# Performance work log

Hardware: AMD Instinct MI355X
Metric: run time of the kernel (lower is better)

Reference implementation:

```python
import jax, jax.numpy as jnp
import numpy as np

N = 50000          # nodes
E = 1000000        # edges (k=20 avg degree)
SD = 32            # scalar_dim = hidden_dim//2
VD = 32            # vector_dim = hidden_dim//2
L = 3              # num_layers
SPIN = 2           # spin_symmetry
IN_DIM = 2 * SD + VD + 3   # message MLP input dim = 99
OUT_DIM = SD + VD          # 64


def setup_inputs() -> dict:
    key = jax.random.key(0)
    ks = jax.random.split(key, 12)
    pos = jax.random.uniform(ks[0], (N, 2), dtype=jnp.float32)
    redshift = jax.random.uniform(ks[1], (N, 1), dtype=jnp.float32)
    input_shapes = jax.random.normal(ks[2], (N, 2), dtype=jnp.float32)
    edge_index = jax.random.randint(ks[3], (2, E), 0, N, dtype=jnp.int64)
    # encoder params
    enc_s_w = jax.random.normal(ks[4], (SD, 1), dtype=jnp.float32) * 0.5
    enc_s_b = jax.random.normal(ks[5], (SD,), dtype=jnp.float32) * 0.1
    enc_v_w = jax.random.normal(ks[6], (VD, 2), dtype=jnp.float32) * 0.5
    # per-layer message MLP params, stacked over layers
    W1 = jax.random.normal(ks[7], (L, OUT_DIM, IN_DIM), dtype=jnp.float32) * (1.0 / np.sqrt(IN_DIM))
    b1 = jax.random.normal(ks[8], (L, OUT_DIM), dtype=jnp.float32) * 0.1
    W2 = jax.random.normal(ks[9], (L, OUT_DIM, OUT_DIM), dtype=jnp.float32) * (1.0 / np.sqrt(OUT_DIM))
    b2 = jax.random.normal(ks[10], (L, OUT_DIM), dtype=jnp.float32) * 0.1
    return {"pos": pos, "redshift": redshift, "input_shapes": input_shapes,
            "edge_index": edge_index, "enc_s_w": enc_s_w, "enc_s_b": enc_s_b,
            "enc_v_w": enc_v_w, "W1": W1, "b1": b1, "W2": W2, "b2": b2}


def _frame_layer(h_s, h_v, pos, orientation, src, dst, W1, b1, W2, b2):
    # per-edge geometric features
    dpos = pos[src] - pos[dst]                                   # [E,2]
    dist = jnp.sqrt(jnp.sum(dpos * dpos, axis=1)) + 1e-6          # [E]
    phi_global = jnp.arctan2(dpos[:, 1], dpos[:, 0])              # [E]
    alpha_i = orientation[dst, 0]                                 # [E]
    delta_phi = phi_global - alpha_i
    geo = jnp.stack([dist, jnp.cos(SPIN * delta_phi), jnp.sin(SPIN * delta_phi)], axis=-1)  # [E,3]
    # rotate source vector features into destination local frame
    beta_j = orientation[src, 0]
    rot = (beta_j - alpha_i) * SPIN
    c, s = jnp.cos(rot)[:, None], jnp.sin(rot)[:, None]           # [E,1]
    v_j = h_v[src].reshape(-1, VD // 2, 2)                        # [E,nv,2]
    vx = v_j[..., 0] * c - v_j[..., 1] * s
    vy = v_j[..., 0] * s + v_j[..., 1] * c
    v_rot = jnp.stack([vx, vy], axis=-1).reshape(-1, VD)          # [E,VD]
    # message MLP
    msg_in = jnp.concatenate([h_s[src], h_s[dst], v_rot, geo], axis=-1)  # [E,IN_DIM]
    hid = jax.nn.silu(msg_in @ W1.T + b1)
    raw = hid @ W2.T + b2                                         # [E,OUT_DIM]
    msg_s, msg_v = raw[:, :SD], raw[:, SD:]
    # scatter-add to destination nodes
    out_s = jax.ops.segment_sum(msg_s, dst, num_segments=h_s.shape[0])
    out_v = jax.ops.segment_sum(msg_v, dst, num_segments=h_v.shape[0])
    return h_s + out_s, h_v + out_v


def reference(pos, redshift, input_shapes, edge_index, enc_s_w, enc_s_b, enc_v_w, W1, b1, W2, b2):
    src, dst = edge_index[0], edge_index[1]
    h_s = jax.nn.relu(redshift @ enc_s_w.T + enc_s_b)             # [N,SD]
    h_v = input_shapes @ enc_v_w.T                                # [N,VD]
    orientation = jnp.zeros((pos.shape[0], 1), dtype=pos.dtype)
    for l in range(L):
        h_s, h_v = _frame_layer(h_s, h_v, pos, orientation, src, dst,
                                W1[l], b1[l], W2[l], b2[l])
    return h_s, h_v
```

## Files before the change

kernel.cpp:

```cpp
#include <hip/hip_runtime.h>
#include <hip/hip_bf16.h>

#define WPB 4
#define TILE 16

typedef unsigned short ushort_t;
typedef unsigned int uint_t;

__device__ __forceinline__ float silu_f(float x) {
  return x * __builtin_amdgcn_rcpf(1.0f + __expf(-x));
}
__device__ __forceinline__ int rfl(int x) { return __builtin_amdgcn_readfirstlane(x); }
__device__ __forceinline__ float readlane_f(float v, int l) {
  return __int_as_float(__builtin_amdgcn_readlane(__float_as_int(v), l));
}
__device__ __forceinline__ ushort_t f2bf(float f) {
  uint_t u = __float_as_uint(f);
  u += 0x7FFFu + ((u >> 16) & 1u);
  return (ushort_t)(u >> 16);
}
__device__ __forceinline__ float bf2f(ushort_t b) {
  return __uint_as_float(((uint_t)b) << 16);
}

__global__ void encode_kernel(const float* __restrict__ redshift,
                              const float* __restrict__ shapes,
                              const float* __restrict__ enc_s_w,
                              const float* __restrict__ enc_s_b,
                              const float* __restrict__ enc_v_w,
                              float* __restrict__ hout, int N_) {
  int tid = blockIdx.x * blockDim.x + threadIdx.x;
  int n = tid >> 5;
  int j = tid & 31;
  if (n >= N_) return;
  float r = redshift[n];
  float hs = fmaxf(fmaf(r, enc_s_w[j], enc_s_b[j]), 0.0f);
  float x0 = shapes[n * 2 + 0];
  float x1 = shapes[n * 2 + 1];
  float hv = fmaf(x0, enc_v_w[j * 2 + 0], x1 * enc_v_w[j * 2 + 1]);
  hout[(size_t)n * 32 + j] = hs;
  hout[(size_t)N_ * 32 + (size_t)n * 32 + j] = hv;
}

__global__ void zero_kernel(int* __restrict__ p, int n) {
  int i = blockIdx.x * blockDim.x + threadIdx.x;
  if (i < n) p[i] = 0;
}

__global__ void deg_kernel(const int* __restrict__ ei, int* __restrict__ deg, int E_) {
  int e = blockIdx.x * blockDim.x + threadIdx.x;
  if (e < E_) atomicAdd(&deg[ei[E_ + e]], 1);
}

__global__ __launch_bounds__(1024) void scanA_kernel(const int* __restrict__ deg,
                                                     int* __restrict__ rowptr,
                                                     int* __restrict__ bsum, int n) {
  __shared__ int wsum[16];
  int t = threadIdx.x, lane = t & 63, wid = t >> 6;
  int i = blockIdx.x * 1024 + t;
  int v = (i < n) ? deg[i] : 0;
  int x = v;
#pragma unroll
  for (int off = 1; off < 64; off <<= 1) {
    int y = __shfl_up(x, off);
    if (lane >= off) x += y;
  }
  if (lane == 63) wsum[wid] = x;
  __syncthreads();
  if (t == 0) {
    int run = 0;
#pragma unroll
    for (int w = 0; w < 16; ++w) { int s = wsum[w]; wsum[w] = run; run += s; }
  }
  __syncthreads();
  int inc = x + wsum[wid];
  if (i < n) rowptr[i + 1] = inc;
  if (t == 1023) bsum[blockIdx.x] = inc;
}

__global__ __launch_bounds__(1024) void scanB_kernel(int* __restrict__ bsum, int nb) {
  __shared__ int wsum[16];
  int t = threadIdx.x, lane = t & 63, wid = t >> 6;
  int v = (t < nb) ? bsum[t] : 0;
  int x = v;
#pragma unroll
  for (int off = 1; off < 64; off <<= 1) {
    int y = __shfl_up(x, off);
    if (lane >= off) x += y;
  }
  if (lane == 63) wsum[wid] = x;
  __syncthreads();
  if (t == 0) {
    int run = 0;
#pragma unroll
    for (int w = 0; w < 16; ++w) { int s = wsum[w]; wsum[w] = run; run += s; }
  }
  __syncthreads();
  if (t < nb) bsum[t] = x - v + wsum[wid];
}

__global__ void scanC_kernel(int* __restrict__ rowptr, const int* __restrict__ bsum, int n) {
  int i = blockIdx.x * blockDim.x + threadIdx.x;
  if (i == 0) rowptr[0] = 0;
  if (i < n) rowptr[i + 1] += bsum[i >> 10];
}

__global__ void scatter_kernel(const int* __restrict__ ei, const float* __restrict__ pos,
                               const int* __restrict__ rowptr, int* __restrict__ cursor,
                               float4* __restrict__ edata, int* __restrict__ dstS,
                               int E_, int padE, int N_) {
  int e = blockIdx.x * blockDim.x + threadIdx.x;
  if (e >= padE) return;
  if (e >= E_) {
    edata[e] = make_float4(0.f, 0.f, 0.f, __int_as_float(0));
    dstS[e] = N_;
    return;
  }
  int s = ei[e];
  int d = ei[E_ + e];
  int idx = rowptr[d] + atomicAdd(&cursor[d], 1);
  float dx = pos[s * 2 + 0] - pos[d * 2 + 0];
  float dy = pos[s * 2 + 1] - pos[d * 2 + 1];
  float r2 = fmaf(dx, dx, dy * dy);
  float dist = sqrtf(r2) + 1e-6f;
  float c2 = 1.0f, s2 = 0.0f;
  if (r2 > 0.0f) {
    float inv = 1.0f / r2;
    c2 = (dx * dx - dy * dy) * inv;
    s2 = 2.0f * dx * dy * inv;
  }
  edata[idx] = make_float4(dist, c2, s2, __int_as_float(s));
  dstS[idx] = d;
}

__global__ __launch_bounds__(256) void psd_kernel(
    const float* __restrict__ hout, const float* __restrict__ W1l,
    const float* __restrict__ b1l,
    ushort_t* __restrict__ PSh, ushort_t* __restrict__ PDBh,
    float* __restrict__ H, int N_) {
  __shared__ float wsh[99 * 64];
  __shared__ __align__(16) float hsh[TILE][64];
  int t = threadIdx.x;
  for (int i = t; i < 99 * 64; i += 256) wsh[i] = W1l[i];
  __syncthreads();
  int lane = t & 63, wib = t >> 6;
  float ws_[32], wd_[32], wv_[32];
#pragma unroll
  for (int k = 0; k < 32; ++k) {
    ws_[k] = wsh[lane * 99 + k];
    wd_[k] = wsh[lane * 99 + 32 + k];
    wv_[k] = wsh[lane * 99 + 64 + k];
  }
  float bb1 = b1l[lane];
  const int nTiles = (N_ + TILE - 1) / TILE;
  const float* hvbase = hout + (size_t)N_ * 32;
  int tt = t & 127;
  int sn = tt >> 3;
  int sc = tt & 7;
  for (int tile = blockIdx.x; tile < nTiles; tile += gridDim.x) {
    int base = tile * TILE;
    {
      int n = base + sn;
      const float* src = (t < 128) ? (hout + (size_t)n * 32 + sc * 4)
                                   : (hvbase + (size_t)n * 32 + sc * 4);
      float4 v = (n < N_) ? *reinterpret_cast<const float4*>(src)
                          : make_float4(0.f, 0.f, 0.f, 0.f);
      *reinterpret_cast<float4*>(&hsh[sn][(t < 128 ? 0 : 32) + sc * 4]) = v;
    }
    __syncthreads();
#pragma unroll
    for (int q = 0; q < 4; ++q) {
      int r = wib + q * 4;
      int n = base + r;
      if (n < N_) {
        const float4* ha = reinterpret_cast<const float4*>(hsh[r]);
        float ps0 = 0.f, ps1 = 0.f, ps2 = 0.f, ps3 = 0.f, pd0 = 0.f, pd1 = 0.f;
#pragma unroll
        for (int k4 = 0; k4 < 8; ++k4) {
          float4 a = ha[k4];
          float4 v = ha[8 + k4];
          int k = k4 * 4;
          ps0 = fmaf(a.x, ws_[k], ps0);     pd0 = fmaf(a.x, wd_[k], pd0);
          ps1 = fmaf(a.y, ws_[k + 1], ps1); pd1 = fmaf(a.y, wd_[k + 1], pd1);
          ps2 = fmaf(a.z, ws_[k + 2], ps2); pd0 = fmaf(a.z, wd_[k + 2], pd0);
          ps3 = fmaf(a.w, ws_[k + 3], ps3); pd1 = fmaf(a.w, wd_[k + 3], pd1);
          ps0 = fmaf(v.x, wv_[k], ps0);
          ps1 = fmaf(v.y, wv_[k + 1], ps1);
          ps2 = fmaf(v.z, wv_[k + 2], ps2);
          ps3 = fmaf(v.w, wv_[k + 3], ps3);
        }
        PSh[(size_t)n * 64 + lane] = f2bf((ps0 + ps1) + (ps2 + ps3));
        PDBh[(size_t)n * 64 + lane] = f2bf((pd0 + pd1) + bb1);
        H[(size_t)n * 64 + lane] = 0.0f;
      }
    }
    __syncthreads();
  }
}

__global__ __launch_bounds__(256) void edge_kernel(
    const ushort_t* __restrict__ PSh, const ushort_t* __restrict__ PDBh,
    const float4* __restrict__ edata, const int* __restrict__ dstS,
    const float* __restrict__ W1l, float* __restrict__ H, int nchunk) {
  int lane = threadIdx.x & 63, wib = threadIdx.x >> 6;
  int chunk = blockIdx.x * WPB + wib;
  if (chunk >= nchunk) return;
  int base = chunk << 6;
  float wg0 = W1l[lane * 99 + 96];
  float wg1 = W1l[lane * 99 + 97];
  float wg2 = W1l[lane * 99 + 98];
  float4 ed = edata[base + lane];
  int dv = dstS[base + lane];
  int sv = __float_as_int(ed.w);
  int dprev = __shfl_up(dv, 1);
  unsigned long long bmask = __ballot(dv != dprev) & ~1ull;
  int dcur = rfl(dv);
  float pdj = bf2f(PDBh[(size_t)dcur * 64 + lane]);
  int bnext = bmask ? (int)__builtin_ctzll(bmask) : 64;
  int dnext = (bnext < 64) ? __builtin_amdgcn_readlane(dv, bnext) : dcur;
  float pdj_next = bf2f(PDBh[(size_t)dnext * 64 + lane]);
  float acc0 = 0.0f, acc1 = 0.0f;
#pragma unroll
  for (int e = 0; e < 64; ++e) {
    if (e == bnext) {
      atomicAdd(H + (size_t)dcur * 64 + lane, acc0 + acc1);
      acc0 = acc1 = 0.0f;
      dcur = dnext;
      pdj = pdj_next;
      bmask &= bmask - 1;
      bnext = bmask ? (int)__builtin_ctzll(bmask) : 64;
      dnext = (bnext < 64) ? __builtin_amdgcn_readlane(dv, bnext) : dcur;
      pdj_next = bf2f(PDBh[(size_t)dnext * 64 + lane]);
    }
    int se = __builtin_amdgcn_readlane(sv, e);
    float di = readlane_f(ed.x, e);
    float c2 = readlane_f(ed.y, e);
    float s2 = readlane_f(ed.z, e);
    float ps = bf2f(PSh[(size_t)se * 64 + lane]);
    float pre = fmaf(wg0, di, fmaf(wg1, c2, fmaf(wg2, s2, ps + pdj)));
    if (e & 1) acc1 += silu_f(pre); else acc0 += silu_f(pre);
  }
  atomicAdd(H + (size_t)dcur * 64 + lane, acc0 + acc1);
}

__global__ __launch_bounds__(256) void updproj_kernel(
    float* __restrict__ hout, float* __restrict__ H,
    const int* __restrict__ deg,
    const float* __restrict__ W2l, const float* __restrict__ b2l,
    const float* __restrict__ W1n, const float* __restrict__ b1n,
    ushort_t* __restrict__ PSh, ushort_t* __restrict__ PDBh, int N_) {
  __shared__ float w2sh[64 * 65];
  __shared__ float wsh[99 * 64];
  __shared__ __align__(16) float Hsh[TILE][64];
  int t = threadIdx.x;
  for (int i = t; i < 64 * 64; i += 256) w2sh[(i >> 6) * 65 + (i & 63)] = W2l[i];
  for (int i = t; i < 99 * 64; i += 256) wsh[i] = W1n[i];
  __syncthreads();
  int lane = t & 63, wib = t >> 6;
  float w2[64];
#pragma unroll
  for (int k = 0; k < 64; ++k) w2[k] = w2sh[lane * 65 + k];
  float ws_[32], wd_[32], wv_[32];
#pragma unroll
  for (int k = 0; k < 32; ++k) {
    ws_[k] = wsh[lane * 99 + k];
    wd_[k] = wsh[lane * 99 + 32 + k];
    wv_[k] = wsh[lane * 99 + 64 + k];
  }
  float bb2 = b2l[lane];
  float bb1 = b1n[lane];
  const int nTiles = (N_ + TILE - 1) / TILE;
  size_t plane = (size_t)(lane >> 5) * ((size_t)N_ * 32);
  int sn = t >> 4;
  int sc = t & 15;
  for (int tile = blockIdx.x; tile < nTiles; tile += gridDim.x) {
    int base = tile * TILE;
    {
      int n = base + sn;
      float4 v = (n < N_) ? *reinterpret_cast<const float4*>(H + (size_t)n * 64 + sc * 4)
                          : make_float4(0.f, 0.f, 0.f, 0.f);
      *reinterpret_cast<float4*>(&Hsh[sn][sc * 4]) = v;
    }
    __syncthreads();
#pragma unroll
    for (int q = 0; q < 4; ++q) {
      int r = wib + q * 4;
      int n = base + r;
      if (n < N_) {
        const float4* hm = reinterpret_cast<const float4*>(Hsh[r]);
        float o0 = 0.f, o1 = 0.f;
#pragma unroll
        for (int k4 = 0; k4 < 16; k4 += 2) {
          float4 m0 = hm[k4];
          float4 m1 = hm[k4 + 1];
          o0 = fmaf(m0.x, w2[k4 * 4 + 0], o0);
          o0 = fmaf(m0.y, w2[k4 * 4 + 1], o0);
          o0 = fmaf(m0.z, w2[k4 * 4 + 2], o0);
          o0 = fmaf(m0.w, w2[k4 * 4 + 3], o0);
          o1 = fmaf(m1.x, w2[k4 * 4 + 4], o1);
          o1 = fmaf(m1.y, w2[k4 * 4 + 5], o1);
          o1 = fmaf(m1.z, w2[k4 * 4 + 6], o1);
          o1 = fmaf(m1.w, w2[k4 * 4 + 7], o1);
        }
        float degf = (float)deg[n];
        size_t idx = plane + (size_t)n * 32 + (lane & 31);
        float hnew = hout[idx] + (o0 + o1) + degf * bb2;
        hout[idx] = hnew;
        Hsh[r][lane] = hnew;
        asm volatile("s_waitcnt lgkmcnt(0)" ::: "memory");
        const float4* ha = reinterpret_cast<const float4*>(Hsh[r]);
        float ps0 = 0.f, ps1 = 0.f, ps2 = 0.f, ps3 = 0.f, pd0 = 0.f, pd1 = 0.f;
#pragma unroll
        for (int k4 = 0; k4 < 8; ++k4) {
          float4 a = ha[k4];
          float4 v = ha[8 + k4];
          int k = k4 * 4;
          ps0 = fmaf(a.x, ws_[k], ps0);     pd0 = fmaf(a.x, wd_[k], pd0);
          ps1 = fmaf(a.y, ws_[k + 1], ps1); pd1 = fmaf(a.y, wd_[k + 1], pd1);
          ps2 = fmaf(a.z, ws_[k + 2], ps2); pd0 = fmaf(a.z, wd_[k + 2], pd0);
          ps3 = fmaf(a.w, ws_[k + 3], ps3); pd1 = fmaf(a.w, wd_[k + 3], pd1);
          ps0 = fmaf(v.x, wv_[k], ps0);
          ps1 = fmaf(v.y, wv_[k + 1], ps1);
          ps2 = fmaf(v.z, wv_[k + 2], ps2);
          ps3 = fmaf(v.w, wv_[k + 3], ps3);
        }
        PSh[(size_t)n * 64 + lane] = f2bf((ps0 + ps1) + (ps2 + ps3));
        PDBh[(size_t)n * 64 + lane] = f2bf((pd0 + pd1) + bb1);
        H[(size_t)n * 64 + lane] = 0.0f;
      }
    }
    __syncthreads();
  }
}

__global__ __launch_bounds__(256) void out_kernel(
    float* __restrict__ hout, const float* __restrict__ H,
    const int* __restrict__ deg,
    const float* __restrict__ W2l, const float* __restrict__ b2l, int N_) {
  __shared__ float w2sh[64 * 65];
  __shared__ __align__(16) float Hsh[TILE][64];
  int t = threadIdx.x;
  for (int i = t; i < 64 * 64; i += 256) w2sh[(i >> 6) * 65 + (i & 63)] = W2l[i];
  __syncthreads();
  int lane = t & 63, wib = t >> 6;
  float w2[64];
#pragma unroll
  for (int k = 0; k < 64; ++k) w2[k] = w2sh[lane * 65 + k];
  float bb2 = b2l[lane];
  const int nTiles = (N_ + TILE - 1) / TILE;
  size_t plane = (size_t)(lane >> 5) * ((size_t)N_ * 32);
  int sn = t >> 4;
  int sc = t & 15;
  for (int tile = blockIdx.x; tile < nTiles; tile += gridDim.x) {
    int base = tile * TILE;
    {
      int n = base + sn;
      float4 v = (n < N_) ? *reinterpret_cast<const float4*>(H + (size_t)n * 64 + sc * 4)
                          : make_float4(0.f, 0.f, 0.f, 0.f);
      *reinterpret_cast<float4*>(&Hsh[sn][sc * 4]) = v;
    }
    __syncthreads();
#pragma unroll
    for (int q = 0; q < 4; ++q) {
      int r = wib + q * 4;
      int n = base + r;
      if (n < N_) {
        const float4* hm = reinterpret_cast<const float4*>(Hsh[r]);
        float o0 = 0.f, o1 = 0.f;
#pragma unroll
        for (int k4 = 0; k4 < 16; k4 += 2) {
          float4 m0 = hm[k4];
          float4 m1 = hm[k4 + 1];
          o0 = fmaf(m0.x, w2[k4 * 4 + 0], o0);
          o0 = fmaf(m0.y, w2[k4 * 4 + 1], o0);
          o0 = fmaf(m0.z, w2[k4 * 4 + 2], o0);
          o0 = fmaf(m0.w, w2[k4 * 4 + 3], o0);
          o1 = fmaf(m1.x, w2[k4 * 4 + 4], o1);
          o1 = fmaf(m1.y, w2[k4 * 4 + 5], o1);
          o1 = fmaf(m1.z, w2[k4 * 4 + 6], o1);
          o1 = fmaf(m1.w, w2[k4 * 4 + 7], o1);
        }
        float degf = (float)deg[n];
        size_t idx = plane + (size_t)n * 32 + (lane & 31);
        hout[idx] += (o0 + o1) + degf * bb2;
      }
    }
    __syncthreads();
  }
}

extern "C" void kernel_launch(void* const* d_in, const int* in_sizes, int n_in,
                              void* d_out, int out_size, void* d_ws, size_t ws_size,
                              hipStream_t stream) {
  const float* pos      = (const float*)d_in[0];
  const float* redshift = (const float*)d_in[1];
  const float* shapes   = (const float*)d_in[2];
  const int*   ei       = (const int*)d_in[3];
  const float* enc_s_w  = (const float*)d_in[4];
  const float* enc_s_b  = (const float*)d_in[5];
  const float* enc_v_w  = (const float*)d_in[6];
  const float* W1       = (const float*)d_in[7];
  const float* b1       = (const float*)d_in[8];
  const float* W2       = (const float*)d_in[9];
  const float* b2       = (const float*)d_in[10];

  const int N_ = in_sizes[1];
  const int E_ = in_sizes[3] / 2;
  const int nchunk = (E_ + 63) / 64;
  const int padE = nchunk * 64;

  float4*   edata = (float4*)d_ws;
  float*    H     = (float*)(edata + padE);
  ushort_t* PSh   = (ushort_t*)(H + (size_t)(N_ + 1) * 64);
  ushort_t* PDBh  = PSh + (size_t)N_ * 64;
  int* dstS   = (int*)(PDBh + (size_t)(N_ + 1) * 64);
  int* rowptr = dstS + padE;
  int* deg    = rowptr + (N_ + 1);
  int* cursor = deg + N_;
  int* bsum   = cursor + N_;

  float* hout = (float*)d_out;

  encode_kernel<<<dim3((N_ * 32 + 255) / 256), dim3(256), 0, stream>>>(
      redshift, shapes, enc_s_w, enc_s_b, enc_v_w, hout, N_);

  zero_kernel<<<dim3((2 * N_ + 255) / 256), dim3(256), 0, stream>>>(deg, 2 * N_);
  deg_kernel<<<dim3((E_ + 255) / 256), dim3(256), 0, stream>>>(ei, deg, E_);
  const int nbA = (N_ + 1023) / 1024;
  scanA_kernel<<<dim3(nbA), dim3(1024), 0, stream>>>(deg, rowptr, bsum, N_);
  scanB_kernel<<<dim3(1), dim3(1024), 0, stream>>>(bsum, nbA);
  scanC_kernel<<<dim3((N_ + 255) / 256), dim3(256), 0, stream>>>(rowptr, bsum, N_);
  scatter_kernel<<<dim3((padE + 255) / 256), dim3(256), 0, stream>>>(
      ei, pos, rowptr, cursor, edata, dstS, E_, padE, N_);

  const int edgeBlocks = (nchunk + WPB - 1) / WPB;

  psd_kernel<<<dim3(1024), dim3(256), 0, stream>>>(
      hout, W1, b1, PSh, PDBh, H, N_);

  for (int l = 0; l < 3; ++l) {
    const float* W2l = W2 + (size_t)l * 64 * 64;
    const float* b2l = b2 + (size_t)l * 64;
    edge_kernel<<<dim3(edgeBlocks), dim3(256), 0, stream>>>(
        PSh, PDBh, edata, dstS, W1 + (size_t)l * 64 * 99, H, nchunk);
    if (l < 2) {
      updproj_kernel<<<dim3(1024), dim3(256), 0, stream>>>(
          hout, H, deg, W2l, b2l,
          W1 + (size_t)(l + 1) * 64 * 99, b1 + (size_t)(l + 1) * 64,
          PSh, PDBh, N_);
    } else {
      out_kernel<<<dim3(1024), dim3(256), 0, stream>>>(
          hout, H, deg, W2l, b2l, N_);
    }
  }
}
```

Baseline: 401.7 us.

## Pack edge data into one float4 and batch source-row gathers by eight

Stores cos/sin of the edge angle as two bf16 values in one word, so the float4 per edge now carries dist, packed trig, source and destination. This removes the separate dstS array and its load in the edge kernel. The edge loop is also restructured to issue eight PSh gathers up front per group, giving more memory-level parallelism. In exchange the angle features lose precision to bf16 and the eight prefetched values raise register pressure.

Measured after the change: 324.7 us. 1.24x faster.

```diff
diff --git a/kernel.cpp b/kernel.cpp
--- a/kernel.cpp
+++ b/kernel.cpp
@@ -107,13 +107,12 @@
 
 __global__ void scatter_kernel(const int* __restrict__ ei, const float* __restrict__ pos,
                                const int* __restrict__ rowptr, int* __restrict__ cursor,
-                               float4* __restrict__ edata, int* __restrict__ dstS,
+                               float4* __restrict__ edata,
                                int E_, int padE, int N_) {
   int e = blockIdx.x * blockDim.x + threadIdx.x;
   if (e >= padE) return;
   if (e >= E_) {
-    edata[e] = make_float4(0.f, 0.f, 0.f, __int_as_float(0));
-    dstS[e] = N_;
+    edata[e] = make_float4(0.f, 0.f, __int_as_float(0), __int_as_float(N_));
     return;
   }
   int s = ei[e];
@@ -129,8 +128,9 @@
     c2 = (dx * dx - dy * dy) * inv;
     s2 = 2.0f * dx * dy * inv;
   }
-  edata[idx] = make_float4(dist, c2, s2, __int_as_float(s));
-  dstS[idx] = d;
+  uint_t pk = ((uint_t)f2bf(s2) << 16) | (uint_t)f2bf(c2);
+  edata[idx] = make_float4(dist, __uint_as_float(pk),
+                           __int_as_float(s), __int_as_float(d));
 }
 
 __global__ __launch_bounds__(256) void psd_kernel(
@@ -200,7 +200,7 @@
 
 __global__ __launch_bounds__(256) void edge_kernel(
     const ushort_t* __restrict__ PSh, const ushort_t* __restrict__ PDBh,
-    const float4* __restrict__ edata, const int* __restrict__ dstS,
+    const float4* __restrict__ edata,
     const float* __restrict__ W1l, float* __restrict__ H, int nchunk) {
   int lane = threadIdx.x & 63, wib = threadIdx.x >> 6;
   int chunk = blockIdx.x * WPB + wib;
@@ -210,8 +210,8 @@
   float wg1 = W1l[lane * 99 + 97];
   float wg2 = W1l[lane * 99 + 98];
   float4 ed = edata[base + lane];
-  int dv = dstS[base + lane];
-  int sv = __float_as_int(ed.w);
+  int sv = __float_as_int(ed.z);
+  int dv = __float_as_int(ed.w);
   int dprev = __shfl_up(dv, 1);
   unsigned long long bmask = __ballot(dv != dprev) & ~1ull;
   int dcur = rfl(dv);
@@ -221,24 +221,49 @@
   float pdj_next = bf2f(PDBh[(size_t)dnext * 64 + lane]);
   float acc0 = 0.0f, acc1 = 0.0f;
 #pragma unroll
-  for (int e = 0; e < 64; ++e) {
-    if (e == bnext) {
-      atomicAdd(H + (size_t)dcur * 64 + lane, acc0 + acc1);
-      acc0 = acc1 = 0.0f;
-      dcur = dnext;
-      pdj = pdj_next;
-      bmask &= bmask - 1;
-      bnext = bmask ? (int)__builtin_ctzll(bmask) : 64;
-      dnext = (bnext < 64) ? __builtin_amdgcn_readlane(dv, bnext) : dcur;
-      pdj_next = bf2f(PDBh[(size_t)dnext * 64 + lane]);
-    }
-    int se = __builtin_amdgcn_readlane(sv, e);
-    float di = readlane_f(ed.x, e);
-    float c2 = readlane_f(ed.y, e);
-    float s2 = readlane_f(ed.z, e);
-    float ps = bf2f(PSh[(size_t)se * 64 + lane]);
-    float pre = fmaf(wg0, di, fmaf(wg1, c2, fmaf(wg2, s2, ps + pdj)));
-    if (e & 1) acc1 += silu_f(pre); else acc0 += silu_f(pre);
+  for (int g = 0; g < 8; ++g) {
+    float ps0, ps1, ps2, ps3, ps4, ps5, ps6, ps7;
+    {
+      int s0 = __builtin_amdgcn_readlane(sv, g * 8 + 0);
+      int s1 = __builtin_amdgcn_readlane(sv, g * 8 + 1);
+      int s2_ = __builtin_amdgcn_readlane(sv, g * 8 + 2);
+      int s3 = __builtin_amdgcn_readlane(sv, g * 8 + 3);
+      int s4 = __builtin_amdgcn_readlane(sv, g * 8 + 4);
+      int s5 = __builtin_amdgcn_readlane(sv, g * 8 + 5);
+      int s6 = __builtin_amdgcn_readlane(sv, g * 8 + 6);
+      int s7 = __builtin_amdgcn_readlane(sv, g * 8 + 7);
+      ps0 = bf2f(PSh[(size_t)s0 * 64 + lane]);
+      ps1 = bf2f(PSh[(size_t)s1 * 64 + lane]);
+      ps2 = bf2f(PSh[(size_t)s2_ * 64 + lane]);
+      ps3 = bf2f(PSh[(size_t)s3 * 64 + lane]);
+      ps4 = bf2f(PSh[(size_t)s4 * 64 + lane]);
+      ps5 = bf2f(PSh[(size_t)s5 * 64 + lane]);
+      ps6 = bf2f(PSh[(size_t)s6 * 64 + lane]);
+      ps7 = bf2f(PSh[(size_t)s7 * 64 + lane]);
+    }
+#pragma unroll
+    for (int i = 0; i < 8; ++i) {
+      int e = g * 8 + i;
+      if (e == bnext) {
+        atomicAdd(H + (size_t)dcur * 64 + lane, acc0 + acc1);
+        acc0 = acc1 = 0.0f;
+        dcur = dnext;
+        pdj = pdj_next;
+        bmask &= bmask - 1;
+        bnext = bmask ? (int)__builtin_ctzll(bmask) : 64;
+        dnext = (bnext < 64) ? __builtin_amdgcn_readlane(dv, bnext) : dcur;
+        pdj_next = bf2f(PDBh[(size_t)dnext * 64 + lane]);
+      }
+      float psv = (i == 0) ? ps0 : (i == 1) ? ps1 : (i == 2) ? ps2 :
+                  (i == 3) ? ps3 : (i == 4) ? ps4 : (i == 5) ? ps5 :
+                  (i == 6) ? ps6 : ps7;
+      float di = readlane_f(ed.x, e);
+      uint_t pk = (uint_t)__builtin_amdgcn_readlane(__float_as_int(ed.y), e);
+      float c2 = __uint_as_float(pk << 16);
+      float s2 = __uint_as_float(pk & 0xFFFF0000u);
+      float pre = fmaf(wg0, di, fmaf(wg1, c2, fmaf(wg2, s2, psv + pdj)));
+      if (e & 1) acc1 += silu_f(pre); else acc0 += silu_f(pre);
+    }
   }
   atomicAdd(H + (size_t)dcur * 64 + lane, acc0 + acc1);
 }
@@ -413,8 +438,7 @@
   float*    H     = (float*)(edata + padE);
   ushort_t* PSh   = (ushort_t*)(H + (size_t)(N_ + 1) * 64);
   ushort_t* PDBh  = PSh + (size_t)N_ * 64;
-  int* dstS   = (int*)(PDBh + (size_t)(N_ + 1) * 64);
-  int* rowptr = dstS + padE;
+  int* rowptr = (int*)(PDBh + (size_t)(N_ + 1) * 64);
   int* deg    = rowptr + (N_ + 1);
   int* cursor = deg + N_;
   int* bsum   = cursor + N_;
@@ -431,7 +455,7 @@
   scanB_kernel<<<dim3(1), dim3(1024), 0, stream>>>(bsum, nbA);
   scanC_kernel<<<dim3((N_ + 255) / 256), dim3(256), 0, stream>>>(rowptr, bsum, N_);
   scatter_kernel<<<dim3((padE + 255) / 256), dim3(256), 0, stream>>>(
-      ei, pos, rowptr, cursor, edata, dstS, E_, padE, N_);
+      ei, pos, rowptr, cursor, edata, E_, padE, N_);
 
   const int edgeBlocks = (nchunk + WPB - 1) / WPB;
 
@@ -442,7 +466,7 @@
     const float* W2l = W2 + (size_t)l * 64 * 64;
     const float* b2l = b2 + (size_t)l * 64;
     edge_kernel<<<dim3(edgeBlocks), dim3(256), 0, stream>>>(
-        PSh, PDBh, edata, dstS, W1 + (size_t)l * 64 * 99, H, nchunk);
+        PSh, PDBh, edata, W1 + (size_t)l * 64 * 99, H, nchunk);
     if (l < 2) {
       updproj_kernel<<<dim3(1024), dim3(256), 0, stream>>>(
           hout, H, deg, W2l, b2l,
```

## Replace CSR build with bucket sort and software-pipeline edge gathers

Applied to the files above, without the earlier changes.

The degree count, three-pass scan and atomic scatter are replaced by a two-level bucket sort. Edges go into fixed-capacity sub-buckets of 256 destination nodes, and each bucket is then sorted locally in shared memory; degrees come from the local histogram. Edge records are packed into one float4 (dist, bf16 cos/sin pair, src, dst), which removes the separate dst array. The edge kernel now issues source-row gathers in double-buffered groups of eight so memory latency overlaps with SiLU accumulation. In exchange, the fixed bucket capacity assumes roughly uniform destinations and could overflow on skewed graphs, and the geometry terms lose precision to bf16.

Measured after the change: 421.7 us. 5.0% more time.

```diff
diff --git a/kernel.cpp b/kernel.cpp
--- a/kernel.cpp
+++ b/kernel.cpp
@@ -3,6 +3,8 @@
 
 #define WPB 4
 #define TILE 16
+#define SUBB 8
+#define BCAP 896
 
 typedef unsigned short ushort_t;
 typedef unsigned int uint_t;
@@ -47,78 +49,13 @@
   if (i < n) p[i] = 0;
 }
 
-__global__ void deg_kernel(const int* __restrict__ ei, int* __restrict__ deg, int E_) {
+__global__ void bucket_kernel(const int* __restrict__ ei, const float* __restrict__ pos,
+                              int* __restrict__ bcnt, float4* __restrict__ bdata,
+                              int E_) {
   int e = blockIdx.x * blockDim.x + threadIdx.x;
-  if (e < E_) atomicAdd(&deg[ei[E_ + e]], 1);
-}
-
-__global__ __launch_bounds__(1024) void scanA_kernel(const int* __restrict__ deg,
-                                                     int* __restrict__ rowptr,
-                                                     int* __restrict__ bsum, int n) {
-  __shared__ int wsum[16];
-  int t = threadIdx.x, lane = t & 63, wid = t >> 6;
-  int i = blockIdx.x * 1024 + t;
-  int v = (i < n) ? deg[i] : 0;
-  int x = v;
-#pragma unroll
-  for (int off = 1; off < 64; off <<= 1) {
-    int y = __shfl_up(x, off);
-    if (lane >= off) x += y;
-  }
-  if (lane == 63) wsum[wid] = x;
-  __syncthreads();
-  if (t == 0) {
-    int run = 0;
-#pragma unroll
-    for (int w = 0; w < 16; ++w) { int s = wsum[w]; wsum[w] = run; run += s; }
-  }
-  __syncthreads();
-  int inc = x + wsum[wid];
-  if (i < n) rowptr[i + 1] = inc;
-  if (t == 1023) bsum[blockIdx.x] = inc;
-}
-
-__global__ __launch_bounds__(1024) void scanB_kernel(int* __restrict__ bsum, int nb) {
-  __shared__ int wsum[16];
-  int t = threadIdx.x, lane = t & 63, wid = t >> 6;
-  int v = (t < nb) ? bsum[t] : 0;
-  int x = v;
-#pragma unroll
-  for (int off = 1; off < 64; off <<= 1) {
-    int y = __shfl_up(x, off);
-    if (lane >= off) x += y;
-  }
-  if (lane == 63) wsum[wid] = x;
-  __syncthreads();
-  if (t == 0) {
-    int run = 0;
-#pragma unroll
-    for (int w = 0; w < 16; ++w) { int s = wsum[w]; wsum[w] = run; run += s; }
-  }
-  __syncthreads();
-  if (t < nb) bsum[t] = x - v + wsum[wid];
-}
-
-__global__ void scanC_kernel(int* __restrict__ rowptr, const int* __restrict__ bsum, int n) {
-  int i = blockIdx.x * blockDim.x + threadIdx.x;
-  if (i == 0) rowptr[0] = 0;
-  if (i < n) rowptr[i + 1] += bsum[i >> 10];
-}
-
-__global__ void scatter_kernel(const int* __restrict__ ei, const float* __restrict__ pos,
-                               const int* __restrict__ rowptr, int* __restrict__ cursor,
-                               float4* __restrict__ edata, int* __restrict__ dstS,
-                               int E_, int padE, int N_) {
-  int e = blockIdx.x * blockDim.x + threadIdx.x;
-  if (e >= padE) return;
-  if (e >= E_) {
-    edata[e] = make_float4(0.f, 0.f, 0.f, __int_as_float(0));
-    dstS[e] = N_;
-    return;
-  }
+  if (e >= E_) return;
   int s = ei[e];
   int d = ei[E_ + e];
-  int idx = rowptr[d] + atomicAdd(&cursor[d], 1);
   float dx = pos[s * 2 + 0] - pos[d * 2 + 0];
   float dy = pos[s * 2 + 1] - pos[d * 2 + 1];
   float r2 = fmaf(dx, dx, dy * dy);
@@ -129,8 +66,85 @@
     c2 = (dx * dx - dy * dy) * inv;
     s2 = 2.0f * dx * dy * inv;
   }
-  edata[idx] = make_float4(dist, c2, s2, __int_as_float(s));
-  dstS[idx] = d;
+  uint_t pk = ((uint_t)f2bf(s2) << 16) | (uint_t)f2bf(c2);
+  int cell = ((d >> 8) << 3) | (blockIdx.x & (SUBB - 1));
+  int slot = atomicAdd(&bcnt[cell], 1);
+  bdata[(size_t)cell * BCAP + slot] =
+      make_float4(dist, __uint_as_float(pk), __int_as_float(s), __int_as_float(d));
+}
+
+__global__ __launch_bounds__(256) void bscan_kernel(const int* __restrict__ bcnt,
+                                                    int* __restrict__ bucketBase, int NB) {
+  __shared__ int wsum[4];
+  int t = threadIdx.x, lane = t & 63, wid = t >> 6;
+  int v = 0;
+  if (t < NB) {
+#pragma unroll
+    for (int x = 0; x < SUBB; ++x) v += bcnt[t * SUBB + x];
+  }
+  int x = v;
+#pragma unroll
+  for (int off = 1; off < 64; off <<= 1) {
+    int y = __shfl_up(x, off);
+    if (lane >= off) x += y;
+  }
+  if (lane == 63) wsum[wid] = x;
+  __syncthreads();
+  if (t == 0) {
+    int run = 0;
+#pragma unroll
+    for (int w = 0; w < 4; ++w) { int s = wsum[w]; wsum[w] = run; run += s; }
+  }
+  __syncthreads();
+  int inc = x + wsum[wid];
+  if (t < NB) bucketBase[t + 1] = inc;
+  if (t == 0) bucketBase[0] = 0;
+}
+
+__global__ __launch_bounds__(256) void bsort_kernel(
+    const float4* __restrict__ bdata, const int* __restrict__ bcnt,
+    const int* __restrict__ bucketBase, float4* __restrict__ edata,
+    int* __restrict__ deg, int N_) {
+  __shared__ int hist[256];
+  __shared__ int offs[256];
+  __shared__ int cur[256];
+  int b = blockIdx.x;
+  int t = threadIdx.x;
+  hist[t] = 0;
+  cur[t] = 0;
+  __syncthreads();
+  for (int x = 0; x < SUBB; ++x) {
+    int cnt = bcnt[b * SUBB + x];
+    const float4* src = bdata + (size_t)(b * SUBB + x) * BCAP;
+    for (int i = t; i < cnt; i += 256) {
+      int d = __float_as_int(src[i].w);
+      atomicAdd(&hist[d & 255], 1);
+    }
+  }
+  __syncthreads();
+  if (t == 0) {
+    int run = 0;
+    for (int i = 0; i < 256; ++i) { offs[i] = run; run += hist[i]; }
+  }
+  __syncthreads();
+  int n = (b << 8) + t;
+  if (n < N_) deg[n] = hist[t];
+  int base = bucketBase[b];
+  for (int x = 0; x < SUBB; ++x) {
+    int cnt = bcnt[b * SUBB + x];
+    const float4* src = bdata + (size_t)(b * SUBB + x) * BCAP;
+    for (int i = t; i < cnt; i += 256) {
+      float4 r = src[i];
+      int ld = __float_as_int(r.w) & 255;
+      int slot = base + offs[ld] + atomicAdd(&cur[ld], 1);
+      edata[slot] = r;
+    }
+  }
+}
+
+__global__ void pad_kernel(float4* __restrict__ edata, int E_, int N_) {
+  int i = E_ + threadIdx.x;
+  edata[i] = make_float4(0.f, 0.f, __int_as_float(0), __int_as_float(N_));
 }
 
 __global__ __launch_bounds__(256) void psd_kernel(
@@ -198,9 +212,61 @@
   }
 }
 
+#define ISSUE(P, G)                                             \
+  do {                                                          \
+    int t0 = __builtin_amdgcn_readlane(sv, (G) + 0);            \
+    int t1 = __builtin_amdgcn_readlane(sv, (G) + 1);            \
+    int t2 = __builtin_amdgcn_readlane(sv, (G) + 2);            \
+    int t3 = __builtin_amdgcn_readlane(sv, (G) + 3);            \
+    int t4 = __builtin_amdgcn_readlane(sv, (G) + 4);            \
+    int t5 = __builtin_amdgcn_readlane(sv, (G) + 5);            \
+    int t6 = __builtin_amdgcn_readlane(sv, (G) + 6);            \
+    int t7 = __builtin_amdgcn_readlane(sv, (G) + 7);            \
+    P##0 = PSh[(size_t)t0 * 64 + lane];                         \
+    P##1 = PSh[(size_t)t1 * 64 + lane];                         \
+    P##2 = PSh[(size_t)t2 * 64 + lane];                         \
+    P##3 = PSh[(size_t)t3 * 64 + lane];                         \
+    P##4 = PSh[(size_t)t4 * 64 + lane];                         \
+    P##5 = PSh[(size_t)t5 * 64 + lane];                         \
+    P##6 = PSh[(size_t)t6 * 64 + lane];                         \
+    P##7 = PSh[(size_t)t7 * 64 + lane];                         \
+  } while (0)
+
+#define FLUSH()                                                          \
+  do {                                                                   \
+    atomicAdd(H + (size_t)dcur * 64 + lane, acc0 + acc1);                \
+    acc0 = acc1 = 0.0f;                                                  \
+    dcur = dnext;                                                        \
+    pdj = pdj_next;                                                      \
+    bmask &= bmask - 1;                                                  \
+    bnext = bmask ? (int)__builtin_ctzll(bmask) : 64;                    \
+    dnext = (bnext < 64) ? __builtin_amdgcn_readlane(dv, bnext) : dcur;  \
+    pdj_next = bf2f(PDBh[(size_t)dnext * 64 + lane]);                    \
+  } while (0)
+
+#define EDGE_ONE(PSV, E)                                                     \
+  do {                                                                       \
+    if ((E) == bnext) FLUSH();                                               \
+    float psv = bf2f((ushort_t)(PSV));                                       \
+    float di = readlane_f(ed.x, (E));                                        \
+    uint_t pk = (uint_t)__builtin_amdgcn_readlane(__float_as_int(ed.y), (E));\
+    float c2 = __uint_as_float(pk << 16);                                    \
+    float s2 = __uint_as_float(pk & 0xFFFF0000u);                            \
+    float pre = fmaf(wg0, di, fmaf(wg1, c2, fmaf(wg2, s2, psv + pdj)));      \
+    if ((E) & 1) acc1 += silu_f(pre); else acc0 += silu_f(pre);              \
+  } while (0)
+
+#define CONSUME(P, G)                                            \
+  do {                                                           \
+    EDGE_ONE(P##0, (G) + 0); EDGE_ONE(P##1, (G) + 1);            \
+    EDGE_ONE(P##2, (G) + 2); EDGE_ONE(P##3, (G) + 3);            \
+    EDGE_ONE(P##4, (G) + 4); EDGE_ONE(P##5, (G) + 5);            \
+    EDGE_ONE(P##6, (G) + 6); EDGE_ONE(P##7, (G) + 7);            \
+  } while (0)
+
 __global__ __launch_bounds__(256) void edge_kernel(
     const ushort_t* __restrict__ PSh, const ushort_t* __restrict__ PDBh,
-    const float4* __restrict__ edata, const int* __restrict__ dstS,
+    const float4* __restrict__ edata,
     const float* __restrict__ W1l, float* __restrict__ H, int nchunk) {
   int lane = threadIdx.x & 63, wib = threadIdx.x >> 6;
   int chunk = blockIdx.x * WPB + wib;
@@ -210,8 +276,8 @@
   float wg1 = W1l[lane * 99 + 97];
   float wg2 = W1l[lane * 99 + 98];
   float4 ed = edata[base + lane];
-  int dv = dstS[base + lane];
-  int sv = __float_as_int(ed.w);
+  int sv = __float_as_int(ed.z);
+  int dv = __float_as_int(ed.w);
   int dprev = __shfl_up(dv, 1);
   unsigned long long bmask = __ballot(dv != dprev) & ~1ull;
   int dcur = rfl(dv);
@@ -220,26 +286,24 @@
   int dnext = (bnext < 64) ? __builtin_amdgcn_readlane(dv, bnext) : dcur;
   float pdj_next = bf2f(PDBh[(size_t)dnext * 64 + lane]);
   float acc0 = 0.0f, acc1 = 0.0f;
-#pragma unroll
-  for (int e = 0; e < 64; ++e) {
-    if (e == bnext) {
-      atomicAdd(H + (size_t)dcur * 64 + lane, acc0 + acc1);
-      acc0 = acc1 = 0.0f;
-      dcur = dnext;
-      pdj = pdj_next;
-      bmask &= bmask - 1;
-      bnext = bmask ? (int)__builtin_ctzll(bmask) : 64;
-      dnext = (bnext < 64) ? __builtin_amdgcn_readlane(dv, bnext) : dcur;
-      pdj_next = bf2f(PDBh[(size_t)dnext * 64 + lane]);
-    }
-    int se = __builtin_amdgcn_readlane(sv, e);
-    float di = readlane_f(ed.x, e);
-    float c2 = readlane_f(ed.y, e);
-    float s2 = readlane_f(ed.z, e);
-    float ps = bf2f(PSh[(size_t)se * 64 + lane]);
-    float pre = fmaf(wg0, di, fmaf(wg1, c2, fmaf(wg2, s2, ps + pdj)));
-    if (e & 1) acc1 += silu_f(pre); else acc0 += silu_f(pre);
-  }
+  uint_t pA0, pA1, pA2, pA3, pA4, pA5, pA6, pA7;
+  uint_t pB0, pB1, pB2, pB3, pB4, pB5, pB6, pB7;
+  ISSUE(pA, 0);
+  ISSUE(pB, 8);
+  CONSUME(pA, 0);
+  ISSUE(pA, 16);
+  CONSUME(pB, 8);
+  ISSUE(pB, 24);
+  CONSUME(pA, 16);
+  ISSUE(pA, 32);
+  CONSUME(pB, 24);
+  ISSUE(pB, 40);
+  CONSUME(pA, 32);
+  ISSUE(pA, 48);
+  CONSUME(pB, 40);
+  ISSUE(pB, 56);
+  CONSUME(pA, 48);
+  CONSUME(pB, 56);
   atomicAdd(H + (size_t)dcur * 64 + lane, acc0 + acc1);
 }
 
@@ -408,30 +472,35 @@
   const int E_ = in_sizes[3] / 2;
   const int nchunk = (E_ + 63) / 64;
   const int padE = nchunk * 64;
-
-  float4*   edata = (float4*)d_ws;
-  float*    H     = (float*)(edata + padE);
-  ushort_t* PSh   = (ushort_t*)(H + (size_t)(N_ + 1) * 64);
-  ushort_t* PDBh  = PSh + (size_t)N_ * 64;
-  int* dstS   = (int*)(PDBh + (size_t)(N_ + 1) * 64);
-  int* rowptr = dstS + padE;
-  int* deg    = rowptr + (N_ + 1);
-  int* cursor = deg + N_;
-  int* bsum   = cursor + N_;
+  const int NB = (N_ + 255) >> 8;
+
+  float4* edata = (float4*)d_ws;
+  char*   regionA = (char*)(edata + padE);
+  float*    H    = (float*)regionA;
+  ushort_t* PSh  = (ushort_t*)(H + (size_t)(N_ + 1) * 64);
+  ushort_t* PDBh = PSh + (size_t)N_ * 64;
+  float4* bdata  = (float4*)regionA;
+  size_t szH = (size_t)(N_ + 1) * 64 * 4 + (size_t)N_ * 64 * 2 + (size_t)(N_ + 1) * 64 * 2;
+  size_t szB = (size_t)NB * SUBB * BCAP * 16;
+  size_t regA = (szH > szB ? szH : szB);
+  regA = (regA + 15) & ~(size_t)15;
+  int* deg        = (int*)(regionA + regA);
+  int* bcnt       = deg + N_;
+  int* bucketBase = bcnt + NB * SUBB;
 
   float* hout = (float*)d_out;
 
   encode_kernel<<<dim3((N_ * 32 + 255) / 256), dim3(256), 0, stream>>>(
       redshift, shapes, enc_s_w, enc_s_b, enc_v_w, hout, N_);
 
-  zero_kernel<<<dim3((2 * N_ + 255) / 256), dim3(256), 0, stream>>>(deg, 2 * N_);
-  deg_kernel<<<dim3((E_ + 255) / 256), dim3(256), 0, stream>>>(ei, deg, E_);
-  const int nbA = (N_ + 1023) / 1024;
-  scanA_kernel<<<dim3(nbA), dim3(1024), 0, stream>>>(deg, rowptr, bsum, N_);
-  scanB_kernel<<<dim3(1), dim3(1024), 0, stream>>>(bsum, nbA);
-  scanC_kernel<<<dim3((N_ + 255) / 256), dim3(256), 0, stream>>>(rowptr, bsum, N_);
-  scatter_kernel<<<dim3((padE + 255) / 256), dim3(256), 0, stream>>>(
-      ei, pos, rowptr, cursor, edata, dstS, E_, padE, N_);
+  zero_kernel<<<dim3((NB * SUBB + 255) / 256), dim3(256), 0, stream>>>(bcnt, NB * SUBB);
+  bucket_kernel<<<dim3((E_ + 255) / 256), dim3(256), 0, stream>>>(
+      ei, pos, bcnt, bdata, E_);
+  bscan_kernel<<<dim3(1), dim3(256), 0, stream>>>(bcnt, bucketBase, NB);
+  bsort_kernel<<<dim3(NB), dim3(256), 0, stream>>>(
+      bdata, bcnt, bucketBase, edata, deg, N_);
+  if (padE > E_)
+    pad_kernel<<<dim3(1), dim3(padE - E_), 0, stream>>>(edata, E_, N_);
 
   const int edgeBlocks = (nchunk + WPB - 1) / WPB;
 
@@ -442,7 +511,7 @@
     const float* W2l = W2 + (size_t)l * 64 * 64;
     const float* b2l = b2 + (size_t)l * 64;
     edge_kernel<<<dim3(edgeBlocks), dim3(256), 0, stream>>>(
-        PSh, PDBh, edata, dstS, W1 + (size_t)l * 64 * 99, H, nchunk);
+        PSh, PDBh, edata, W1 + (size_t)l * 64 * 99, H, nchunk);
     if (l < 2) {
       updproj_kernel<<<dim3(1024), dim3(256), 0, stream>>>(
           hout, H, deg, W2l, b2l,
```
